# Kernel optimization log

Measured on AMD Instinct MI355X. Metric: run time of the kernel, lower is better.

The kernel has to match this reference:

```python
import jax, jax.numpy as jnp
import numpy as np

VOCAB = 50000
EMB = 300
HID = 300
LAYERS = 2
NTAGS = 11  # tags 0..8 are real labels, 9=START, 10=STOP
START = NTAGS - 2
STOP = NTAGS - 1
NEG = -10000.0


def _lstm_params(key, in_dim, hid):
    k = 1.0 / np.sqrt(hid)
    ks = jax.random.split(key, 4)
    u = lambda kk, shp: jax.random.uniform(kk, shp, jnp.float32, -k, k)
    return {
        'Wi': u(ks[0], (4 * hid, in_dim)),
        'Wh': u(ks[1], (4 * hid, hid)),
        'bi': u(ks[2], (4 * hid,)),
        'bh': u(ks[3], (4 * hid,)),
    }


def _run_lstm(p, xs, reverse=False):
    # xs: [T, B, D] -> [T, B, H]
    B = xs.shape[1]
    H = p['Wh'].shape[1]
    pre = jnp.einsum('tbd,gd->tbg', xs, p['Wi']) + p['bi'] + p['bh']

    def step(carry, pre_t):
        h, c = carry
        g = pre_t + h @ p['Wh'].T
        i, f, gg, o = jnp.split(g, 4, axis=-1)
        i = jax.nn.sigmoid(i)
        f = jax.nn.sigmoid(f)
        gg = jnp.tanh(gg)
        o = jax.nn.sigmoid(o)
        c = f * c + i * gg
        h = o * jnp.tanh(c)
        return (h, c), h

    init = (jnp.zeros((B, H), xs.dtype), jnp.zeros((B, H), xs.dtype))
    _, hs = jax.lax.scan(step, init, pre, reverse=reverse)
    return hs


def setup_inputs() -> dict:
    key = jax.random.key(0)
    ks = jax.random.split(key, 12)
    x = jax.random.randint(ks[0], (64, 512), 0, VOCAB, dtype=jnp.int32)
    emb = jax.random.normal(ks[1], (VOCAB, EMB), jnp.float32) * 0.02
    lstm = []
    ki = 2
    for layer in range(LAYERS):
        in_dim = EMB if layer == 0 else 2 * HID
        fwd = _lstm_params(ks[ki], in_dim, HID); ki += 1
        bwd = _lstm_params(ks[ki], in_dim, HID); ki += 1
        lstm.append((fwd, bwd))
    Wout = jax.random.normal(ks[ki], (NTAGS, 2 * HID), jnp.float32) * 0.02
    bout = jnp.zeros((NTAGS,), jnp.float32)
    trans = jax.random.normal(ks[ki + 1], (NTAGS, NTAGS), jnp.float32) * 0.1
    # transitions[i, j] = score of transitioning TO i FROM j
    trans = trans.at[START, :].set(NEG).at[:, STOP].set(NEG)
    params = {'emb': emb, 'Wout': Wout, 'bout': bout, 'trans': trans}
    for li, (f, b) in enumerate(lstm):
        for nm, d in (('f', f), ('b', b)):
            for k2, v in d.items():
                params[f'l{li}{nm}_{k2}'] = v
    return {'x': x, **params}


def _features(x, params):
    h = params['emb'][x]  # [B,T,E]
    h = jnp.transpose(h, (1, 0, 2))  # [T,B,E]
    for li in range(LAYERS):
        pf = {k2: params[f'l{li}f_{k2}'] for k2 in ('Wi', 'Wh', 'bi', 'bh')}
        pb = {k2: params[f'l{li}b_{k2}'] for k2 in ('Wi', 'Wh', 'bi', 'bh')}
        hf = _run_lstm(pf, h)
        hb = _run_lstm(pb, h, reverse=True)
        h = jnp.concatenate([hf, hb], axis=-1)  # [T,B,2H]
    feats = jnp.einsum('tbh,gh->tbg', h, params['Wout']) + params['bout']
    return feats  # [T,B,NTAGS]


def _viterbi(feats, trans):
    # feats: [T,B,K]; trans[i,j]: to i from j
    T, B, K = feats.shape
    init = jnp.full((B, K), NEG, feats.dtype).at[:, START].set(0.0)

    def step(fv, feat_t):
        # scores[b, i, j] = fv[b, j] + trans[i, j]
        scores = fv[:, None, :] + trans[None, :, :]
        bp = jnp.argmax(scores, axis=-1)  # [B,K]
        fv_new = jnp.max(scores, axis=-1) + feat_t
        return fv_new, bp

    fv, bps = jax.lax.scan(step, init, feats)  # bps: [T,B,K]
    term = fv + trans[STOP][None, :]
    best_last = jnp.argmax(term, axis=-1)  # [B]
    path_score = jnp.max(term, axis=-1)

    def back(tag, bp_t):
        prev = jnp.take_along_axis(bp_t, tag[:, None], axis=-1)[:, 0]
        return prev, tag

    _, path = jax.lax.scan(back, best_last, bps, reverse=True)  # [T,B]
    return path_score, jnp.transpose(path)  # [B], [B,T]


def reference(x, emb, Wout, bout, trans,
              l0f_Wi, l0f_Wh, l0f_bi, l0f_bh, l0b_Wi, l0b_Wh, l0b_bi, l0b_bh,
              l1f_Wi, l1f_Wh, l1f_bi, l1f_bh, l1b_Wi, l1b_Wh, l1b_bi, l1b_bh):
    params = dict(emb=emb, Wout=Wout, bout=bout, trans=trans,
                  l0f_Wi=l0f_Wi, l0f_Wh=l0f_Wh, l0f_bi=l0f_bi, l0f_bh=l0f_bh,
                  l0b_Wi=l0b_Wi, l0b_Wh=l0b_Wh, l0b_bi=l0b_bi, l0b_bh=l0b_bh,
                  l1f_Wi=l1f_Wi, l1f_Wh=l1f_Wh, l1f_bi=l1f_bi, l1f_bh=l1f_bh,
                  l1b_Wi=l1b_Wi, l1b_Wh=l1b_Wh, l1b_bi=l1b_bi, l1b_bh=l1b_bh)
    feats = _features(x, params)
    path_score, path = _viterbi(feats, trans)
    return path_score, path
```

## Files before the change

kernel.cpp:

```cpp
#include <hip/hip_runtime.h>
#include <hip/hip_bf16.h>

#define T_SEQ 512
#define NBATCH 64
#define HID 300
#define G4 1200
#define NTAG 11
#define TAG_START 9
#define TAG_STOP 10
#define NEGV -10000.0f
#define NWGD 38
#define NKT 10
#define HXE (40*2*64*8)
#define FLGS 16
#define FLGN 152
#define FLGDIR (FLGN*FLGS)
#define SSTEP 16
#define NCOMP 80

typedef unsigned short u16;
using short8 = __attribute__((ext_vector_type(8))) short;
using f32x4  = __attribute__((ext_vector_type(4))) float;
using f32x16 = __attribute__((ext_vector_type(16))) float;
using i32x4  = __attribute__((ext_vector_type(4))) int;

#define MF(a, b, c)   __builtin_amdgcn_mfma_f32_16x16x32_bf16((a), (b), (c), 0, 0, 0)
#define MF32(a, b, c) __builtin_amdgcn_mfma_f32_32x32x16_bf16((a), (b), (c), 0, 0, 0)

__device__ __forceinline__ float sigf(float x) { return 1.0f / (1.0f + expf(-x)); }

__device__ __forceinline__ u16 f2bf(float x) {
    unsigned u = __float_as_uint(x);
    unsigned r = (u + 0x7FFFu + ((u >> 16) & 1u)) >> 16;
    return (u16)r;
}
__device__ __forceinline__ float bf2f(u16 h) {
    return __uint_as_float((unsigned)h << 16);
}
__device__ __forceinline__ f32x16 zero16() {
    f32x16 z = {0.f,0.f,0.f,0.f,0.f,0.f,0.f,0.f,0.f,0.f,0.f,0.f,0.f,0.f,0.f,0.f};
    return z;
}

__device__ __forceinline__ i32x4 ld_cc_x4(const u16* p) {
    i32x4 r;
    asm volatile("global_load_dwordx4 %0, %1, off sc0 sc1" : "=v"(r) : "v"(p) : "memory");
    return r;
}
__device__ __forceinline__ unsigned ld_cc_b32(const unsigned* p) {
    unsigned r;
    asm volatile("global_load_dword %0, %1, off sc0 sc1\n\t"
                 "s_waitcnt vmcnt(0)" : "=v"(r) : "v"(p) : "memory");
    return r;
}
__device__ __forceinline__ void st_cc_x4(u16* p, i32x4 v) {
    asm volatile("global_store_dwordx4 %0, %1, off sc0 sc1" :: "v"(p), "v"(v) : "memory");
}
__device__ __forceinline__ void st_cc_b32(unsigned* p, unsigned v) {
    asm volatile("global_store_dword %0, %1, off sc0 sc1" :: "v"(p), "v"(v) : "memory");
}
__device__ __forceinline__ void wait_vm0() {
    asm volatile("s_waitcnt vmcnt(0)" ::: "memory");
}

__global__ __launch_bounds__(256) void k_gather(const int* __restrict__ x,
                                                const float* __restrict__ emb,
                                                u16* __restrict__ xs0)
{
    int t = blockIdx.x;
    __shared__ int rid[NBATCH];
    if (threadIdx.x < NBATCH) rid[threadIdx.x] = x[threadIdx.x * T_SEQ + t];
    __syncthreads();
    for (int o = threadIdx.x; o < 64 * 40; o += 256) {
        int b = o / 40, m8 = o - b * 40;
        unsigned hw[4], lw[4];
#pragma unroll
        for (int p = 0; p < 4; ++p) {
            int k0 = m8 * 8 + p * 2;
            float v0 = (k0 < 300)     ? emb[(size_t)rid[b] * 300 + k0]     : 0.0f;
            float v1 = (k0 + 1 < 300) ? emb[(size_t)rid[b] * 300 + k0 + 1] : 0.0f;
            u16 h0 = f2bf(v0), h1 = f2bf(v1);
            u16 l0 = f2bf(v0 - bf2f(h0)), l1 = f2bf(v1 - bf2f(h1));
            hw[p] = (unsigned)h0 | ((unsigned)h1 << 16);
            lw[p] = (unsigned)l0 | ((unsigned)l1 << 16);
        }
        u16* dst = xs0 + (((size_t)t * 40 + m8) * 64 + b) * 16;
        *(i32x4*)dst       = i32x4{(int)hw[0], (int)hw[1], (int)hw[2], (int)hw[3]};
        *(i32x4*)(dst + 8) = i32x4{(int)lw[0], (int)lw[1], (int)lw[2], (int)lw[3]};
    }
}

__global__ __launch_bounds__(256) void k_zpad(u16* __restrict__ xs1)
{
    int t = blockIdx.x;
    i32x4* base = (i32x4*)(xs1 + (((size_t)t * 80 + 76) * 64) * 16);
    i32x4 z = {0, 0, 0, 0};
    for (int o = threadIdx.x; o < 4 * 64 * 2; o += 256) base[o] = z;
}

template<int KMAXW>
__device__ __forceinline__ void pregemm3_role(
    const u16* __restrict__ xs, int TNB,
    const float* __restrict__ Wi,
    float* __restrict__ pre,
    int jquad, int dir, int B0, int KOFF,
    int t0f, int t0b, int s0, int s1, int tid)
{
    const int NKS = 20;
    int wv = tid >> 6, l = tid & 63;
    int jb = jquad * 4 + wv;
    int lo5 = l & 31, hi5 = l >> 5;

    short8 aH2[NKS], aL2[NKS];
    {
        int g = lo5 & 3, uo = lo5 >> 2;
        int jrow = jb * 8 + uo;
        bool jok = jrow < 300;
        const float* wr = Wi + ((size_t)g * 300 + (jok ? jrow : 0)) * KMAXW + KOFF;
#pragma unroll
        for (int ks = 0; ks < NKS; ++ks) {
            short8 vh, vl;
#pragma unroll
            for (int e = 0; e < 8; ++e) {
                int u = ks * 16 + hi5 * 8 + e;
                float w = (jok && u < 300) ? wr[u] : 0.0f;
                u16 hb = f2bf(w);
                vh[e] = (short)hb;
                vl[e] = (short)f2bf(w - bf2f(hb));
            }
            aH2[ks] = vh; aL2[ks] = vl;
        }
    }

    for (int s = s0; s < s1; ++s) {
        int t = dir ? (t0b - s) : (t0f + s);
        const u16* bt = xs + (((size_t)t * TNB + B0) * 64) * 16;
        float* po = pre + (size_t)s * (G4 * 64);
#pragma unroll
        for (int bh2 = 0; bh2 < 2; ++bh2) {
            int bcol = bh2 * 32 + lo5;
            f32x16 aA = zero16(), aB = zero16(), aC = zero16();
#pragma unroll
            for (int ks = 0; ks < NKS; ++ks) {
                const u16* gp = bt + ((size_t)(2 * ks + hi5) * 64 + bcol) * 16;
                short8 bhv = *(const short8*)gp;
                short8 blv = *(const short8*)(gp + 8);
                aA = MF32(aH2[ks], bhv, aA);
                aB = MF32(aL2[ks], bhv, aB);
                aC = MF32(aH2[ks], blv, aC);
            }
#pragma unroll
            for (int r = 0; r < 16; ++r) {
                int m = (r & 3) + 8 * (r >> 2) + 4 * hi5;
                int gg = m & 3, u2 = m >> 2;
                int jr = jb * 8 + u2;
                if (jr < 300)
                    po[(gg * 300 + jr) * 64 + bcol] = aA[r] + aB[r] + aC[r];
            }
        }
    }
}

template<int KMAXW>
__global__ __launch_bounds__(256, 1) void k_pregemm3(
    const u16* __restrict__ xs, int TNB,
    const float* __restrict__ WiF, const float* __restrict__ WiB,
    float* __restrict__ pbase, unsigned long long Q,
    int t0f, int t0b, int NSL, int C)
{
    int bx = blockIdx.x;
    int u = bx / NSL, sl = bx - u * NSL;
    int dir = u & 1, rest = u >> 1;
    int seg = (rest >= 10) ? 1 : 0;
    int jq = rest - seg * 10;
    int s0 = sl * SSTEP, s1 = min(s0 + SSTEP, C);
    pregemm3_role<KMAXW>(xs, TNB, dir ? WiB : WiF,
        pbase + (size_t)(seg * 2 + dir) * Q, jq, dir, seg * 38, seg * 300,
        t0f, t0b, s0, s1, threadIdx.x);
}

template<int MODE>
__device__ __forceinline__ void lstm_role(
    const float* __restrict__ pc, unsigned long long Qc,
    const float* __restrict__ WhF, const float* __restrict__ WhB,
    const float* __restrict__ biF, const float* __restrict__ bhF,
    const float* __restrict__ biB, const float* __restrict__ bhB,
    u16* __restrict__ hx, float* __restrict__ cbuf,
    float* __restrict__ xs2, u16* __restrict__ xs1,
    int t0f, int t0b, int C, int first,
    unsigned* __restrict__ flags,
    volatile unsigned* wgprog,
    int bid, int tid)
{
    __builtin_amdgcn_s_setprio(1);
    int dir = bid & 1, idx = bid >> 1;
    const float* pre  = pc + (size_t)dir * Qc;
    const float* pre2 = pc + (size_t)(2 + dir) * Qc;
    const float* Wh  = dir ? WhB : WhF;
    const float* biL = dir ? biB : biF;
    const float* bhL = dir ? bhB : bhF;
    u16* hxd = hx + (size_t)dir * 2 * HXE;
    float* cb = cbuf + (size_t)dir * 300 * 64;
    unsigned* flg = flags + (size_t)dir * FLGDIR;
    int w = tid >> 6, l = tid & 63;
    int hh = l >> 4, kbx = l >> 4;
    int bcol = w * 16 + (l & 15);
    int j0 = idx * 8;
    int ju0 = j0 + hh, ju1 = j0 + 4 + hh;
    int jc0 = min(ju0, 299), jc1 = min(ju1, 299);
    bool jv0 = ju0 < 300, jv1 = ju1 < 300;

    unsigned* myflag = flg + (size_t)(idx * 4 + w) * FLGS;
    const unsigned* shardp = flg + (size_t)(w * 38 + min(l, 37)) * FLGS;
    bool shact = l < 38;

    if (l == 0) wgprog[w] = 0;
    __syncthreads();

    short8 aH[2][NKT], aL[2][NKT];
    {
        int r = l & 15;
        int g = r & 3, uo = r >> 2;
#pragma unroll
        for (int q = 0; q < 2; ++q) {
            int jr = j0 + q * 4 + uo;
            const float* wr = Wh + ((size_t)g * 300 + min(jr, 299)) * 300;
            bool jvr = jr < 300;
#pragma unroll
            for (int kt = 0; kt < NKT; ++kt) {
                short8 vh, vl;
#pragma unroll
                for (int e = 0; e < 8; ++e) {
                    int k = kt * 32 + kbx * 8 + e;
                    float wv = (jvr && k < 300) ? wr[k] : 0.0f;
                    u16 hb = f2bf(wv);
                    vh[e] = (short)hb;
                    vl[e] = (short)f2bf(wv - bf2f(hb));
                }
                aH[q][kt] = vh; aL[q][kt] = vl;
            }
        }
    }
    float c0 = first ? 0.0f : cb[(size_t)jc0 * 64 + bcol];
    float c1 = first ? 0.0f : cb[(size_t)jc1 * 64 + bcol];

    float bias0[4], bias1[4];
#pragma unroll
    for (int g = 0; g < 4; ++g) {
        bias0[g] = biL[g * 300 + jc0] + bhL[g * 300 + jc0];
        bias1[g] = biL[g * 300 + jc1] + bhL[g * 300 + jc1];
    }

    float p0[4], p1[4];
#pragma unroll
    for (int g = 0; g < 4; ++g) {
        size_t o0 = ((size_t)g * 300 + jc0) * 64 + bcol;
        size_t o1 = ((size_t)g * 300 + jc1) * 64 + bcol;
        p0[g] = pre[o0] + bias0[g];
        p1[g] = pre[o1] + bias1[g];
        if (MODE == 0) { p0[g] += pre2[o0]; p1[g] += pre2[o1]; }
    }

    int pp = 0;
    for (int s = 0; s < C; ++s) {
        f32x4 aA0 = {0.f,0.f,0.f,0.f}, aB0 = {0.f,0.f,0.f,0.f}, aC0 = {0.f,0.f,0.f,0.f};
        f32x4 aA1 = {0.f,0.f,0.f,0.f}, aB1 = {0.f,0.f,0.f,0.f}, aC1 = {0.f,0.f,0.f,0.f};
        if (!(first && s == 0)) {
            const u16* hxr = hxd + (size_t)pp * HXE;
            i32x4 bh[NKT], bl[NKT];
#pragma unroll
            for (int kt = 0; kt < NKT; ++kt) {
                const u16* gp = hxr + (size_t)(4 * kt + kbx) * 1024 + (size_t)bcol * 8;
                bh[kt] = ld_cc_x4(gp);
            }
#pragma unroll
            for (int kt = 0; kt < NKT; ++kt) {
                const u16* gp = hxr + (size_t)(4 * kt + kbx) * 1024 + (size_t)bcol * 8;
                bl[kt] = ld_cc_x4(gp + 512);
            }
            asm volatile("s_waitcnt vmcnt(10)" ::: "memory");
            __builtin_amdgcn_sched_barrier(0);
#pragma unroll
            for (int kt = 0; kt < NKT; ++kt) {
                short8 bhv = __builtin_bit_cast(short8, bh[kt]);
                aA0 = MF(aH[0][kt], bhv, aA0);
                aB0 = MF(aL[0][kt], bhv, aB0);
                aA1 = MF(aH[1][kt], bhv, aA1);
                aB1 = MF(aL[1][kt], bhv, aB1);
            }
            wait_vm0();
            __builtin_amdgcn_sched_barrier(0);
#pragma unroll
            for (int kt = 0; kt < NKT; ++kt) {
                short8 blv = __builtin_bit_cast(short8, bl[kt]);
                aC0 = MF(aH[0][kt], blv, aC0);
                aC1 = MF(aH[1][kt], blv, aC1);
            }
        }
        float hv0, hv1;
        {
            float gi = sigf(aA0[0] + aB0[0] + aC0[0] + p0[0]);
            float gf = sigf(aA0[1] + aB0[1] + aC0[1] + p0[1]);
            float gg = tanhf(aA0[2] + aB0[2] + aC0[2] + p0[2]);
            float go = sigf(aA0[3] + aB0[3] + aC0[3] + p0[3]);
            c0 = gf * c0 + gi * gg;
            hv0 = go * tanhf(c0);
            if (!jv0) hv0 = 0.0f;
        }
        {
            float gi = sigf(aA1[0] + aB1[0] + aC1[0] + p1[0]);
            float gf = sigf(aA1[1] + aB1[1] + aC1[1] + p1[1]);
            float gg = tanhf(aA1[2] + aB1[2] + aC1[2] + p1[2]);
            float go = sigf(aA1[3] + aB1[3] + aC1[3] + p1[3]);
            c1 = gf * c1 + gi * gg;
            hv1 = go * tanhf(c1);
            if (!jv1) hv1 = 0.0f;
        }
        u16 hb0 = f2bf(hv0);
        unsigned pk0 = (unsigned)hb0 | ((unsigned)f2bf(hv0 - bf2f(hb0)) << 16);
        u16 hb1 = f2bf(hv1);
        unsigned pk1 = (unsigned)hb1 | ((unsigned)f2bf(hv1 - bf2f(hb1)) << 16);
        int ls = l & 15;
        unsigned a0 = __shfl(pk0, ls), a1 = __shfl(pk0, ls + 16), a2 = __shfl(pk0, ls + 32), a3 = __shfl(pk0, ls + 48);
        unsigned b0 = __shfl(pk1, ls), b1 = __shfl(pk1, ls + 16), b2 = __shfl(pk1, ls + 32), b3 = __shfl(pk1, ls + 48);
        i32x4 hi4 = {(int)((a0 & 0xffffu) | (a1 << 16)), (int)((a2 & 0xffffu) | (a3 << 16)),
                     (int)((b0 & 0xffffu) | (b1 << 16)), (int)((b2 & 0xffffu) | (b3 << 16))};
        i32x4 lo4 = {(int)((a0 >> 16) | (a1 & 0xffff0000u)), (int)((a2 >> 16) | (a3 & 0xffff0000u)),
                     (int)((b0 >> 16) | (b1 & 0xffff0000u)), (int)((b2 >> 16) | (b3 & 0xffff0000u))};
        int t = dir ? (t0b - s) : (t0f + s);
        if (l < 16) {
            int b = w * 16 + l;
            u16* hxw = hxd + (size_t)(pp ^ 1) * HXE + (size_t)idx * 1024 + (size_t)b * 8;
            st_cc_x4(hxw, hi4);
            st_cc_x4(hxw + 512, lo4);
        }
        wait_vm0();
        if (l == 0) st_cc_b32(myflag, (unsigned)(s + 1));
        if (MODE == 0) {
            if (jv0) xs2[((size_t)t * 600 + dir * 300 + ju0) * 64 + bcol] = hv0;
            if (jv1) xs2[((size_t)t * 600 + dir * 300 + ju1) * 64 + bcol] = hv1;
        } else if (l < 16) {
            int b = w * 16 + l;
            u16* xd = xs1 + (((size_t)t * 80 + dir * 38 + idx) * 64 + b) * 16;
            *(i32x4*)xd       = hi4;
            *(i32x4*)(xd + 8) = lo4;
        }
        if (s + 1 < C) {
#pragma unroll
            for (int g = 0; g < 4; ++g) {
                size_t o0 = ((size_t)(s + 1) * G4 + (size_t)g * 300 + jc0) * 64 + bcol;
                size_t o1 = ((size_t)(s + 1) * G4 + (size_t)g * 300 + jc1) * 64 + bcol;
                p0[g] = pre[o0] + bias0[g];
                p1[g] = pre[o1] + bias1[g];
                if (MODE == 0) { p0[g] += pre2[o0]; p1[g] += pre2[o1]; }
            }
            unsigned tgt = (unsigned)(s + 1);
            unsigned ok;
            do {
                unsigned v = tgt;
                if (shact) v = ld_cc_b32(shardp);
                ok = (v >= tgt) ? 1u : 0u;
            } while (!__all(ok));
            if (l == 0) wgprog[w] = tgt;
            while (!(wgprog[0] >= tgt && wgprog[1] >= tgt &&
                     wgprog[2] >= tgt && wgprog[3] >= tgt)) {
                __builtin_amdgcn_s_sleep(1);
            }
        }
        pp ^= 1;
    }
    if (jv0) cb[(size_t)jc0 * 64 + bcol] = c0;
    if (jv1) cb[(size_t)jc1 * 64 + bcol] = c1;
}

template<int KMAXW, int MODE>
__global__ __launch_bounds__(256, 1) void k_chunk(
    const u16* __restrict__ xsN, int TNB,
    const float* __restrict__ WiF, const float* __restrict__ WiB,
    float* __restrict__ pn, unsigned long long Qn,
    int t0fN, int t0bN, int do_pre, int CN, int NSLc,
    const float* __restrict__ pc, unsigned long long Qc,
    const float* __restrict__ WhF, const float* __restrict__ WhB,
    const float* __restrict__ biF, const float* __restrict__ bhF,
    const float* __restrict__ biB, const float* __restrict__ bhB,
    u16* __restrict__ hx, float* __restrict__ cbuf,
    float* __restrict__ xs2, u16* __restrict__ xs1,
    int t0f, int t0b, int C, int first,
    unsigned* __restrict__ flags)
{
    __shared__ unsigned wgprog[4];
    int bid = blockIdx.x;
    if (bid < 2 * NWGD) {
        lstm_role<MODE>(pc, Qc, WhF, WhB, biF, bhF, biB, bhB, hx, cbuf,
                        xs2, xs1, t0f, t0b, C, first, flags, wgprog,
                        bid, threadIdx.x);
    } else if (do_pre) {
        const int NUNITS = (MODE == 0) ? 40 : 20;
        int p = bid - 2 * NWGD;
        if (p < NUNITS * NSLc) {
            int u = p / NSLc, sl = p - u * NSLc;
            int dir = u & 1, rest = u >> 1;
            int seg = (rest >= 10) ? 1 : 0;
            int jq = rest - seg * 10;
            int s0 = sl * SSTEP, s1 = min(s0 + SSTEP, CN);
            pregemm3_role<KMAXW>(xsN, TNB, dir ? WiB : WiF,
                pn + (size_t)(seg * 2 + dir) * Qn, jq, dir, seg * 38, seg * 300,
                t0fN, t0bN, s0, s1, threadIdx.x);
        }
    }
}

__global__ __launch_bounds__(256) void k_feats(
    const float* __restrict__ xs2, const float* __restrict__ Wout,
    const float* __restrict__ bout, float* __restrict__ feats)
{
    int t = blockIdx.x;
    int tid = threadIdx.x;
    int b = tid & 63, g0 = tid >> 6;
    const float* xa = xs2 + (size_t)t * 600 * 64 + b;
    for (int g = g0; g < NTAG; g += 4) {
        float acc = bout[g];
        const float* wr = Wout + (size_t)g * 600;
#pragma unroll 4
        for (int k = 0; k < 600; ++k) acc += wr[k] * xa[(size_t)k * 64];
        feats[((size_t)t * NTAG + g) * 64 + b] = acc;
    }
}

__global__ __launch_bounds__(256) void k_viterbi(
    const float* __restrict__ feats, const float* __restrict__ trans,
    float* __restrict__ out)
{
    __shared__ unsigned char bp[4][T_SEQ * NTAG];
    int tid = threadIdx.x;
    int wv = tid >> 6, lane = tid & 63;
    int b = blockIdx.x * 4 + wv;
    int i = (lane < NTAG) ? lane : 0;
    bool act = lane < NTAG;
    float trow[NTAG];
#pragma unroll
    for (int j = 0; j < NTAG; ++j) trow[j] = trans[i * NTAG + j];
    float fv = (lane == TAG_START) ? 0.0f : NEGV;
    for (int t = 0; t < T_SEQ; ++t) {
        float m = -3.0e38f; int arg = 0;
#pragma unroll
        for (int j = 0; j < NTAG; ++j) {
            float fvj = __shfl(fv, j, 64);
            float sc = fvj + trow[j];
            if (sc > m) { m = sc; arg = j; }
        }
        float ft = feats[((size_t)t * NTAG + i) * 64 + b];
        fv = m + ft;
        if (act) bp[wv][t * NTAG + lane] = (unsigned char)arg;
    }
    float term = act ? (fv + trans[TAG_STOP * NTAG + i]) : -3.0e38f;
    int bi_ = lane;
#pragma unroll
    for (int off = 32; off >= 1; off >>= 1) {
        float ov = __shfl_xor(term, off, 64);
        int oi = __shfl_xor(bi_, off, 64);
        if (ov > term || (ov == term && oi < bi_)) { term = ov; bi_ = oi; }
    }
    if (lane == 0) {
        out[b] = term;
        int tag = bi_;
        float* po = out + 64 + (size_t)b * T_SEQ;
        for (int t = T_SEQ - 1; t >= 0; --t) {
            po[t] = (float)tag;
            tag = bp[wv][t * NTAG + tag];
        }
    }
}

extern "C" void kernel_launch(void* const* d_in, const int* in_sizes, int n_in,
                              void* d_out, int out_size, void* d_ws, size_t ws_size,
                              hipStream_t stream)
{
    (void)in_sizes; (void)n_in; (void)out_size;
    const int*   x     = (const int*)d_in[0];
    const float* emb   = (const float*)d_in[1];
    const float* Wout  = (const float*)d_in[2];
    const float* bout  = (const float*)d_in[3];
    const float* trans = (const float*)d_in[4];

    float* ws = (float*)d_ws;
    const size_t XS2F = (size_t)T_SEQ * 600 * NBATCH;
    const size_t XS1U = (size_t)T_SEQ * 80 * 64 * 16;
    const size_t FEA  = (size_t)T_SEQ * NTAG * NBATCH;

    float* xs2 = ws;
    u16* xs0 = (u16*)ws;
    u16* xs1 = (u16*)(ws + XS2F);
    float* featB = (float*)(xs1 + XS1U);
    float* cB = featB + FEA;
    u16* hxB = (u16*)(cB + 2 * 300 * 64);
    unsigned* flagsB = (unsigned*)(hxB + 4 * HXE);
    unsigned* padB = flagsB + 64ULL * 2 * FLGDIR;
    float* preBase = (float*)(padB + 16);
    size_t fixedBytes = (size_t)((char*)preBase - (char*)ws);

    int Cmax = 512;
    while (Cmax > 16 && fixedBytes + 16ULL * Cmax * G4 * NBATCH > ws_size) Cmax >>= 1;
    if (Cmax > 64) Cmax = 64;
    int Cmax1 = Cmax >> 1;
    size_t Q0 = (size_t)Cmax  * G4 * NBATCH;
    size_t Q1 = (size_t)Cmax1 * G4 * NBATCH;
    size_t slotF = 2 * Q0;
    float* preS[2] = { preBase, preBase + slotF };

    (void)hipMemsetAsync(hxB, 0,
        4 * HXE * sizeof(u16) + (64ULL * 2 * FLGDIR) * sizeof(unsigned), stream);
    k_gather<<<T_SEQ, 256, 0, stream>>>(x, emb, xs0);
    k_zpad<<<T_SEQ, 256, 0, stream>>>(xs1);

    for (int layer = 0; layer < 2; ++layer) {
        int base = 5 + layer * 8;
        const float* WiF = (const float*)d_in[base + 0];
        const float* WhF = (const float*)d_in[base + 1];
        const float* biF = (const float*)d_in[base + 2];
        const float* bhF = (const float*)d_in[base + 3];
        const float* WiB = (const float*)d_in[base + 4];
        const float* WhB = (const float*)d_in[base + 5];
        const float* biB = (const float*)d_in[base + 6];
        const float* bhB = (const float*)d_in[base + 7];
        const u16* xsL = (layer == 0) ? xs0 : xs1;
        int TNB = (layer == 0) ? 40 : 80;
        int NSEG = (layer == 0) ? 1 : 2;
        int CmaxL = (layer == 0) ? Cmax : Cmax1;
        size_t QL = (layer == 0) ? Q0 : Q1;

        int sizes[40], off[41], nch = 0;
        {
            int rem = T_SEQ;
            int f = (CmaxL >= 64) ? 32 : CmaxL;
            sizes[nch++] = f; rem -= f;
            while (rem > 0) { int s = rem < CmaxL ? rem : CmaxL; sizes[nch++] = s; rem -= s; }
            off[0] = 0;
            for (int i = 0; i < nch; ++i) off[i + 1] = off[i] + sizes[i];
        }

        {
            int NSL0 = (sizes[0] + SSTEP - 1) / SSTEP;
            if (layer == 0)
                k_pregemm3<300><<<NSEG * 20 * NSL0, 256, 0, stream>>>(
                    xsL, TNB, WiF, WiB, preS[0], QL, 0, T_SEQ - 1, NSL0, sizes[0]);
            else
                k_pregemm3<600><<<NSEG * 20 * NSL0, 256, 0, stream>>>(
                    xsL, TNB, WiF, WiB, preS[0], QL, 0, T_SEQ - 1, NSL0, sizes[0]);
        }

        for (int ci = 0; ci < nch; ++ci) {
            int cur = ci & 1, nxt = cur ^ 1;
            int t0f = off[ci], t0b = (T_SEQ - 1) - off[ci];
            int do_pre = (ci + 1 < nch) ? 1 : 0;
            int CN = do_pre ? sizes[ci + 1] : 0;
            int NSLc = do_pre ? (CN + SSTEP - 1) / SSTEP : 1;
            int t0fN = off[ci + 1], t0bN = (T_SEQ - 1) - off[ci + 1];
            int slot = layer * 32 + ci;
            unsigned* flags = flagsB + (size_t)slot * 2 * FLGDIR;
            float* pc = preS[cur];
            float* pn = preS[nxt];
            if (layer == 0)
                k_chunk<300, 1><<<2 * NWGD + NCOMP, 256, 0, stream>>>(
                    xsL, TNB, WiF, WiB, pn, QL, t0fN, t0bN, do_pre, CN, NSLc,
                    pc, QL, WhF, WhB, biF, bhF, biB, bhB, hxB, cB,
                    xs2, xs1, t0f, t0b, sizes[ci], (ci == 0) ? 1 : 0, flags);
            else
                k_chunk<600, 0><<<2 * NWGD + NCOMP, 256, 0, stream>>>(
                    xsL, TNB, WiF, WiB, pn, QL, t0fN, t0bN, do_pre, CN, NSLc,
                    pc, QL, WhF, WhB, biF, bhF, biB, bhB, hxB, cB,
                    xs2, xs1, t0f, t0b, sizes[ci], (ci == 0) ? 1 : 0, flags);
        }
    }
    k_feats<<<T_SEQ, 256, 0, stream>>>(xs2, Wout, bout, featB);
    k_viterbi<<<16, 256, 0, stream>>>(featB, trans, (float*)d_out);
}
```

Measured before the change: 6.410 ms.

## Pace next-chunk input GEMM workers against LSTM progress flags

Inside the chunk kernel, the next chunk's input-projection GEMM no longer uses many short slice blocks. Each of a fixed set of blocks (40 units) now walks the whole chunk, and before each step it reads an LSTM workgroup's progress flag and waits until the recurrence has advanced proportionally, minus a slack. The aim is to stop the GEMM blocks from competing with the latency-critical recurrent workgroups for memory and compute bandwidth, spreading the work across the chunk instead of bursting at the start. The risk is that fewer GEMM blocks and the spin-waits leave the next chunk's pre-activations unfinished when the recurrence ends, which would stretch the critical path.

```diff
diff --git a/kernel.cpp b/kernel.cpp
--- a/kernel.cpp
+++ b/kernel.cpp
@@ -16,7 +16,8 @@
 #define FLGN 152
 #define FLGDIR (FLGN*FLGS)
 #define SSTEP 16
-#define NCOMP 80
+#define NCOMP 40
+#define PSLACK 8
 
 typedef unsigned short u16;
 using short8 = __attribute__((ext_vector_type(8))) short;
@@ -104,12 +105,14 @@
     const float* __restrict__ Wi,
     float* __restrict__ pre,
     int jquad, int dir, int B0, int KOFF,
-    int t0f, int t0b, int s0, int s1, int tid)
+    int t0f, int t0b, int s0, int s1, int tid,
+    const unsigned* __restrict__ paceb, int Ccur)
 {
     const int NKS = 20;
     int wv = tid >> 6, l = tid & 63;
     int jb = jquad * 4 + wv;
     int lo5 = l & 31, hi5 = l >> 5;
+    const unsigned* pace = paceb ? (paceb + (size_t)wv * FLGS) : nullptr;
 
     short8 aH2[NKS], aL2[NKS];
     {
@@ -132,7 +135,20 @@
         }
     }
 
+    unsigned lastv = 0;
     for (int s = s0; s < s1; ++s) {
+        if (pace) {
+            int need = (int)(((long long)s * Ccur) / s1) - PSLACK;
+            if (need > 0 && (int)lastv < need) {
+                unsigned v = 0;
+                do {
+                    if (l == 0) v = ld_cc_b32(pace);
+                    v = __shfl(v, 0);
+                    if ((int)v < need) __builtin_amdgcn_s_sleep(16);
+                } while ((int)v < need);
+                lastv = v;
+            }
+        }
         int t = dir ? (t0b - s) : (t0f + s);
         const u16* bt = xs + (((size_t)t * TNB + B0) * 64) * 16;
         float* po = pre + (size_t)s * (G4 * 64);
@@ -176,7 +192,7 @@
     int s0 = sl * SSTEP, s1 = min(s0 + SSTEP, C);
     pregemm3_role<KMAXW>(xs, TNB, dir ? WiB : WiF,
         pbase + (size_t)(seg * 2 + dir) * Q, jq, dir, seg * 38, seg * 300,
-        t0f, t0b, s0, s1, threadIdx.x);
+        t0f, t0b, s0, s1, threadIdx.x, nullptr, 0);
 }
 
 template<int MODE>
@@ -378,7 +394,7 @@
     const u16* __restrict__ xsN, int TNB,
     const float* __restrict__ WiF, const float* __restrict__ WiB,
     float* __restrict__ pn, unsigned long long Qn,
-    int t0fN, int t0bN, int do_pre, int CN, int NSLc,
+    int t0fN, int t0bN, int do_pre, int CN,
     const float* __restrict__ pc, unsigned long long Qc,
     const float* __restrict__ WhF, const float* __restrict__ WhB,
     const float* __restrict__ biF, const float* __restrict__ bhF,
@@ -397,15 +413,15 @@
     } else if (do_pre) {
         const int NUNITS = (MODE == 0) ? 40 : 20;
         int p = bid - 2 * NWGD;
-        if (p < NUNITS * NSLc) {
-            int u = p / NSLc, sl = p - u * NSLc;
-            int dir = u & 1, rest = u >> 1;
+        if (p < NUNITS) {
+            int dir = p & 1, rest = p >> 1;
             int seg = (rest >= 10) ? 1 : 0;
             int jq = rest - seg * 10;
-            int s0 = sl * SSTEP, s1 = min(s0 + SSTEP, CN);
+            unsigned* flg = flags + (size_t)dir * FLGDIR;
+            const unsigned* paceb = flg + (size_t)((rest * 3) % 38) * 4 * FLGS;
             pregemm3_role<KMAXW>(xsN, TNB, dir ? WiB : WiF,
                 pn + (size_t)(seg * 2 + dir) * Qn, jq, dir, seg * 38, seg * 300,
-                t0fN, t0bN, s0, s1, threadIdx.x);
+                t0fN, t0bN, 0, CN, threadIdx.x, paceb, C);
         }
     }
 }
@@ -554,7 +570,6 @@
             int t0f = off[ci], t0b = (T_SEQ - 1) - off[ci];
             int do_pre = (ci + 1 < nch) ? 1 : 0;
             int CN = do_pre ? sizes[ci + 1] : 0;
-            int NSLc = do_pre ? (CN + SSTEP - 1) / SSTEP : 1;
             int t0fN = off[ci + 1], t0bN = (T_SEQ - 1) - off[ci + 1];
             int slot = layer * 32 + ci;
             unsigned* flags = flagsB + (size_t)slot * 2 * FLGDIR;
@@ -562,12 +577,12 @@
             float* pn = preS[nxt];
             if (layer == 0)
                 k_chunk<300, 1><<<2 * NWGD + NCOMP, 256, 0, stream>>>(
-                    xsL, TNB, WiF, WiB, pn, QL, t0fN, t0bN, do_pre, CN, NSLc,
+                    xsL, TNB, WiF, WiB, pn, QL, t0fN, t0bN, do_pre, CN,
                     pc, QL, WhF, WhB, biF, bhF, biB, bhB, hxB, cB,
                     xs2, xs1, t0f, t0b, sizes[ci], (ci == 0) ? 1 : 0, flags);
             else
                 k_chunk<600, 0><<<2 * NWGD + NCOMP, 256, 0, stream>>>(
-                    xsL, TNB, WiF, WiB, pn, QL, t0fN, t0bN, do_pre, CN, NSLc,
+                    xsL, TNB, WiF, WiB, pn, QL, t0fN, t0bN, do_pre, CN,
                     pc, QL, WhF, WhB, biF, bhF, biB, bhB, hxB, cB,
                     xs2, xs1, t0f, t0b, sizes[ci], (ci == 0) ? 1 : 0, flags);
         }
```

Result: slower. 13.52 ms (+110.9%).

## Run next-chunk input GEMM as separate kernel instead of co-scheduled in LSTM launch

Applied to the files above, without the earlier changes.

Removes the extra workgroups that computed the next chunk's input projection alongside the recurrent LSTM workgroups in one launch. The input projection now runs as a standalone k_pregemm3 launch between chunk kernels, with a smaller slice step so it spreads over more workgroups. This drops the overlap of pre-GEMM with the latency-bound recurrence, so that work now sits serially on the critical path. In exchange the recurrent kernel no longer shares the GPU with GEMM blocks that compete for bandwidth and caches, and the pre-GEMM gets the whole device.

```diff
diff --git a/kernel.cpp b/kernel.cpp
--- a/kernel.cpp
+++ b/kernel.cpp
@@ -15,8 +15,7 @@
 #define FLGS 16
 #define FLGN 152
 #define FLGDIR (FLGN*FLGS)
-#define SSTEP 16
-#define NCOMP 80
+#define SSTEP 8
 
 typedef unsigned short u16;
 using short8 = __attribute__((ext_vector_type(8))) short;
@@ -373,12 +372,8 @@
     if (jv1) cb[(size_t)jc1 * 64 + bcol] = c1;
 }
 
-template<int KMAXW, int MODE>
+template<int MODE>
 __global__ __launch_bounds__(256, 1) void k_chunk(
-    const u16* __restrict__ xsN, int TNB,
-    const float* __restrict__ WiF, const float* __restrict__ WiB,
-    float* __restrict__ pn, unsigned long long Qn,
-    int t0fN, int t0bN, int do_pre, int CN, int NSLc,
     const float* __restrict__ pc, unsigned long long Qc,
     const float* __restrict__ WhF, const float* __restrict__ WhB,
     const float* __restrict__ biF, const float* __restrict__ bhF,
@@ -389,25 +384,9 @@
     unsigned* __restrict__ flags)
 {
     __shared__ unsigned wgprog[4];
-    int bid = blockIdx.x;
-    if (bid < 2 * NWGD) {
-        lstm_role<MODE>(pc, Qc, WhF, WhB, biF, bhF, biB, bhB, hx, cbuf,
-                        xs2, xs1, t0f, t0b, C, first, flags, wgprog,
-                        bid, threadIdx.x);
-    } else if (do_pre) {
-        const int NUNITS = (MODE == 0) ? 40 : 20;
-        int p = bid - 2 * NWGD;
-        if (p < NUNITS * NSLc) {
-            int u = p / NSLc, sl = p - u * NSLc;
-            int dir = u & 1, rest = u >> 1;
-            int seg = (rest >= 10) ? 1 : 0;
-            int jq = rest - seg * 10;
-            int s0 = sl * SSTEP, s1 = min(s0 + SSTEP, CN);
-            pregemm3_role<KMAXW>(xsN, TNB, dir ? WiB : WiF,
-                pn + (size_t)(seg * 2 + dir) * Qn, jq, dir, seg * 38, seg * 300,
-                t0fN, t0bN, s0, s1, threadIdx.x);
-        }
-    }
+    lstm_role<MODE>(pc, Qc, WhF, WhB, biF, bhF, biB, bhB, hx, cbuf,
+                    xs2, xs1, t0f, t0b, C, first, flags, wgprog,
+                    blockIdx.x, threadIdx.x);
 }
 
 __global__ __launch_bounds__(256) void k_feats(
@@ -552,24 +531,30 @@
         for (int ci = 0; ci < nch; ++ci) {
             int cur = ci & 1, nxt = cur ^ 1;
             int t0f = off[ci], t0b = (T_SEQ - 1) - off[ci];
-            int do_pre = (ci + 1 < nch) ? 1 : 0;
-            int CN = do_pre ? sizes[ci + 1] : 0;
-            int NSLc = do_pre ? (CN + SSTEP - 1) / SSTEP : 1;
-            int t0fN = off[ci + 1], t0bN = (T_SEQ - 1) - off[ci + 1];
             int slot = layer * 32 + ci;
             unsigned* flags = flagsB + (size_t)slot * 2 * FLGDIR;
             float* pc = preS[cur];
-            float* pn = preS[nxt];
             if (layer == 0)
-                k_chunk<300, 1><<<2 * NWGD + NCOMP, 256, 0, stream>>>(
-                    xsL, TNB, WiF, WiB, pn, QL, t0fN, t0bN, do_pre, CN, NSLc,
+                k_chunk<1><<<2 * NWGD, 256, 0, stream>>>(
                     pc, QL, WhF, WhB, biF, bhF, biB, bhB, hxB, cB,
                     xs2, xs1, t0f, t0b, sizes[ci], (ci == 0) ? 1 : 0, flags);
             else
-                k_chunk<600, 0><<<2 * NWGD + NCOMP, 256, 0, stream>>>(
-                    xsL, TNB, WiF, WiB, pn, QL, t0fN, t0bN, do_pre, CN, NSLc,
+                k_chunk<0><<<2 * NWGD, 256, 0, stream>>>(
                     pc, QL, WhF, WhB, biF, bhF, biB, bhB, hxB, cB,
                     xs2, xs1, t0f, t0b, sizes[ci], (ci == 0) ? 1 : 0, flags);
+
+            if (ci + 1 < nch) {
+                int CN = sizes[ci + 1];
+                int NSLn = (CN + SSTEP - 1) / SSTEP;
+                int t0fN = off[ci + 1], t0bN = (T_SEQ - 1) - off[ci + 1];
+                float* pn = preS[nxt];
+                if (layer == 0)
+                    k_pregemm3<300><<<NSEG * 20 * NSLn, 256, 0, stream>>>(
+                        xsL, TNB, WiF, WiB, pn, QL, t0fN, t0bN, NSLn, CN);
+                else
+                    k_pregemm3<600><<<NSEG * 20 * NSLn, 256, 0, stream>>>(
+                        xsL, TNB, WiF, WiB, pn, QL, t0fN, t0bN, NSLn, CN);
+            }
         }
     }
     k_feats<<<T_SEQ, 256, 0, stream>>>(xs2, Wout, bout, featB);
```

Result: slower. 7.576 ms (+18.2%).
